# Kernel optimization log

Hardware: AMD Instinct MI355X
Metric: run time of the kernel (lower is better)

Reference implementation:

```python
import jax, jax.numpy as jnp
import numpy as np

B, T, S, C = 4096, 128, 16, 128
NEG = -1e30  # finite stand-in for -inf to keep grads NaN-free


def setup_inputs() -> dict:
    key = jax.random.key(0)
    k1, k2 = jax.random.split(key)
    prediction = jax.random.normal(k1, (B, T, C), dtype=jnp.float32)  # treated as log-probs, as in the original
    lable = jax.random.normal(k2, (B, S, C), dtype=jnp.float32)       # one-hot-ish label scores
    return {"prediction": prediction, "lable": lable}


def _ctc_nll(logp, targets):
    """CTC negative log-likelihood, full-length inputs/targets.
    logp: (B, T, C) log-probabilities, blank=0. targets: (B, S) int.
    Returns nll: (B,)."""
    Bb, Tt, Cc = logp.shape
    Ss = targets.shape[1]
    L = 2 * Ss + 1  # extended label: blank-interleaved
    neg = jnp.float32(NEG)

    ext = jnp.zeros((Bb, L), dtype=targets.dtype).at[:, 1::2].set(targets)
    # skip transition l-2 -> l allowed iff ext[l] != ext[l-2] (auto-false on blanks)
    skip_ok = jnp.concatenate(
        [jnp.zeros((Bb, 2), dtype=bool), ext[:, 2:] != ext[:, :-2]], axis=1)

    # gather log-probs of extended labels for every time step: (B, T, L)
    logp_ext = jnp.take_along_axis(logp, ext[:, None, :], axis=2)

    alpha0 = (jnp.full((Bb, L), neg)
              .at[:, 0].set(logp_ext[:, 0, 0])
              .at[:, 1].set(logp_ext[:, 0, 1]))

    pad1 = jnp.full((Bb, 1), neg)
    pad2 = jnp.full((Bb, 2), neg)

    def step(alpha, lp_t):
        a1 = alpha
        a2 = jnp.concatenate([pad1, alpha[:, :-1]], axis=1)
        a3 = jnp.where(skip_ok, jnp.concatenate([pad2, alpha[:, :-2]], axis=1), neg)
        alpha_new = jnp.logaddexp(jnp.logaddexp(a1, a2), a3) + lp_t
        return alpha_new, None

    alpha_T, _ = jax.lax.scan(step, alpha0, jnp.swapaxes(logp_ext, 0, 1)[1:])
    nll = -jnp.logaddexp(alpha_T[:, -1], alpha_T[:, -2])
    return nll


def reference(prediction, lable):
    # synthesize_lable: per-(b,s) argmax over classes -> integer targets (B, S)
    targets = jnp.argmax(lable, axis=-1)
    nll = _ctc_nll(prediction, targets)
    # zero_infinity=True
    nll = jnp.where(jnp.isfinite(nll), nll, jnp.float32(0.0))
    # reduction='mean': divide each loss by its target length, then batch-mean
    Ss = lable.shape[1]
    return jnp.mean(nll / jnp.float32(Ss))
```

## Files before the change

### kernel.cpp

```cpp
#include <hip/hip_runtime.h>
#include <math.h>
#include <stdint.h>

#define B_ 4096
#define T_ 128
#define S_ 16
#define C_ 128
#define L_ 33
#define NSLOT 17
#define NELEM (T_ * NSLOT)
#define LDSF  (NELEM + 64)
#define NWAVE 2048
#define NEGV (-1e30f)
#define LOG2E 1.4426950408889634f
#define LN2 0.6931471805599453f
#define NEGB (NEGV * LOG2E)

__device__ __forceinline__ float hexp2(float x) { return __builtin_amdgcn_exp2f(x); }
__device__ __forceinline__ float hlog2(float x) { return __builtin_amdgcn_logf(x); }

__device__ __forceinline__ unsigned fkey(float v) {
    unsigned u = __float_as_uint(v);
    return (u & 0x80000000u) ? ~u : (u | 0x80000000u);
}

typedef const __attribute__((address_space(1))) unsigned int* gas_t;
typedef __attribute__((address_space(3))) unsigned int* las_t;

__global__ __launch_bounds__(256) void ctc_main_kernel(
        const float* __restrict__ pred,
        const float* __restrict__ lab,
        float* __restrict__ out_b) {
    const int wid  = threadIdx.x >> 6;
    const int lane = threadIdx.x & 63;
    const int w = blockIdx.x * 4 + wid;
    const int b0 = w, b1 = w + NWAVE;

    __shared__ int   cls_tab[4][NSLOT];
    __shared__ float lps[4][LDSF];
    int*   mytab = cls_tab[wid];
    float* mylds = lps[wid];

    const int half = lane >> 5;
    const int li   = lane & 31;

    const int l = lane;
    int cidx = 0;
    if (l < L_ && (l & 1)) cidx = 1 + ((l - 1) >> 1);
    const bool has2 = (l >= 1);
    const bool odd3 = (l < L_ && (l & 1) && l >= 3);

    float4 q[8];
    auto load_lab = [&](int b) {
        const float4* lr = (const float4*)(lab + (size_t)b * S_ * C_ + (size_t)half * C_);
        #pragma unroll
        for (int sp = 0; sp < 8; ++sp)
            q[sp] = lr[(size_t)sp * 2 * (C_ / 4) + li];
    };
    auto argmax_tab = [&]() {
        if (lane == 0) mytab[0] = 0;
        #pragma unroll
        for (int sp = 0; sp < 8; ++sp) {
            float vals[4] = {q[sp].x, q[sp].y, q[sp].z, q[sp].w};
            unsigned long long key = 0;
            #pragma unroll
            for (int k = 0; k < 4; ++k) {
                unsigned long long kk =
                    ((unsigned long long)fkey(vals[k]) << 32) | (unsigned)(~(li * 4 + k));
                if (kk > key) key = kk;
            }
            #pragma unroll
            for (int off = 16; off >= 1; off >>= 1) {
                unsigned long long ok = __shfl_xor(key, off, 64);
                if (ok > key) key = ok;
            }
            if (li == 0) mytab[1 + sp * 2 + half] = (int)(~(unsigned)key) & 127;
        }
        asm volatile("s_waitcnt lgkmcnt(0)" ::: "memory");
    };
    auto stage = [&](const float* pb, int i0, int i1) {
        for (int i = i0; i < i1; ++i) {
            unsigned e = i * 64 + lane;
            unsigned t = e / NSLOT;
            unsigned s = e - t * NSLOT;
            const float* src = pb + (size_t)t * C_ + mytab[s];
            __builtin_amdgcn_global_load_lds((gas_t)src, (las_t)(mylds + i * 64), 4, 0, 0);
        }
        __builtin_amdgcn_sched_barrier(0);
    };

    float beta, lpA, lpB, lpC;
    bool skipv;
    auto ring_init = [&]() {
        beta = (l <= 1) ? mylds[cidx] * LOG2E : NEGB;
        lpA = mylds[1 * NSLOT + cidx];
        lpB = mylds[2 * NSLOT + cidx];
        lpC = mylds[3 * NSLOT + cidx];
    };
#define SEG(T0, T1)                                                         \
    _Pragma("unroll 4")                                                     \
    for (int t = (T0); t <= (T1); ++t) {                                    \
        float lp = lpA; lpA = lpB; lpB = lpC;                               \
        lpC = mylds[(t + 3) * NSLOT + cidx];                                \
        float a2 = __shfl_up(beta, 1, 64);                                  \
        float a3 = __shfl_up(beta, 2, 64);                                  \
        a2 = has2  ? a2 : NEGB;                                             \
        a3 = skipv ? a3 : NEGB;                                             \
        float m = fmaxf(fmaxf(beta, a2), a3);                               \
        float s = hexp2(beta - m) + hexp2(a2 - m) + hexp2(a3 - m);          \
        beta = fmaf(lp, LOG2E, m + hlog2(s));                               \
    }
    auto finish = [&](int b) {
        float b31 = __shfl(beta, L_ - 2, 64);
        float b32 = __shfl(beta, L_ - 1, 64);
        float m2 = fmaxf(b31, b32);
        float nll = -(m2 + hlog2(hexp2(b31 - m2) + hexp2(b32 - m2))) * LN2;
        if (!isfinite(nll)) nll = 0.0f;
        if (lane == 0) out_b[b] = nll * (1.0f / (float)S_);
    };

    const float* pb0 = pred + (size_t)b0 * T_ * C_;
    const float* pb1 = pred + (size_t)b1 * T_ * C_;

    load_lab(b0);
    asm volatile("s_waitcnt vmcnt(0)" ::: "memory");
    argmax_tab();
    bool skip0 = odd3 && (mytab[cidx] != mytab[cidx - 1]);
    stage(pb0, 0, 17);
    stage(pb0, 17, 34);
    load_lab(b1);
    __builtin_amdgcn_sched_barrier(0);

    asm volatile("s_waitcnt vmcnt(25)" ::: "memory");
    ring_init();
    skipv = skip0;
    SEG(1, 60)

    asm volatile("s_waitcnt vmcnt(0)" ::: "memory");
    argmax_tab();
    bool skip1 = odd3 && (mytab[cidx] != mytab[cidx - 1]);
    stage(pb1, 0, 17);
    SEG(61, 127)
    finish(b0);

    stage(pb1, 17, 34);
    asm volatile("s_waitcnt vmcnt(17)" ::: "memory");
    ring_init();
    skipv = skip1;
    SEG(1, 60)

    asm volatile("s_waitcnt vmcnt(0)" ::: "memory");
    SEG(61, 127)
    finish(b1);
#undef SEG
}

__global__ __launch_bounds__(256) void reduce_mean_kernel(
        const float* __restrict__ in, float* __restrict__ out) {
    __shared__ float sm[256];
    const int tid = threadIdx.x;
    float v[16];
    #pragma unroll
    for (int i = 0; i < 16; ++i) v[i] = in[tid + i * 256];
    float s = 0.f;
    #pragma unroll
    for (int i = 0; i < 16; ++i) s += v[i];
    sm[tid] = s;
    __syncthreads();
    for (int w = 128; w >= 1; w >>= 1) {
        if (tid < w) sm[tid] += sm[tid + w];
        __syncthreads();
    }
    if (tid == 0) out[0] = sm[0] / (float)B_;
}

extern "C" void kernel_launch(void* const* d_in, const int* in_sizes, int n_in,
                              void* d_out, int out_size, void* d_ws, size_t ws_size,
                              hipStream_t stream) {
    const float* pred = (const float*)d_in[0];
    const float* lab  = (const float*)d_in[1];
    float* ws = (float*)d_ws;
    ctc_main_kernel<<<NWAVE / 4, 256, 0, stream>>>(pred, lab, ws);
    reduce_mean_kernel<<<1, 256, 0, stream>>>(ws, (float*)d_out);
}
```

Baseline: 65.81 us.

## Process one batch per wave with double-buffered chunked LDS staging

Each wave now handles a single batch instead of two, which doubles the grid to 4096 waves and raises per-SIMD occupancy for the latency-bound serial alpha recurrence. The full per-batch gathered log-prob table in LDS is replaced by a two-region ring of 32-timestep chunks, staged ahead of the compute loop. This roughly halves LDS per wave and permits launch_bounds(256,8). The trade-off is losing the old overlap of the second batch's label argmax and staging with the first batch's recurrence, and adding more per-chunk waitcnt points.

Measured after the change: 61.76 us. 1.07x faster.

```diff
diff --git a/kernel.cpp b/kernel.cpp
--- a/kernel.cpp
+++ b/kernel.cpp
@@ -8,9 +8,10 @@
 #define C_ 128
 #define L_ 33
 #define NSLOT 17
-#define NELEM (T_ * NSLOT)
-#define LDSF  (NELEM + 64)
-#define NWAVE 2048
+#define CH_ROWS 32
+#define CH_FLOATS 544
+#define REG_FLOATS 544
+#define LDS_FLOATS 1120
 #define NEGV (-1e30f)
 #define LOG2E 1.4426950408889634f
 #define LN2 0.6931471805599453f
@@ -27,41 +28,38 @@
 typedef const __attribute__((address_space(1))) unsigned int* gas_t;
 typedef __attribute__((address_space(3))) unsigned int* las_t;
 
-__global__ __launch_bounds__(256) void ctc_main_kernel(
+__global__ __launch_bounds__(256, 8) void ctc_main_kernel(
         const float* __restrict__ pred,
         const float* __restrict__ lab,
         float* __restrict__ out_b) {
     const int wid  = threadIdx.x >> 6;
     const int lane = threadIdx.x & 63;
-    const int w = blockIdx.x * 4 + wid;
-    const int b0 = w, b1 = w + NWAVE;
+    const int b = blockIdx.x * 4 + wid;
 
     __shared__ int   cls_tab[4][NSLOT];
-    __shared__ float lps[4][LDSF];
+    __shared__ float lps[4][LDS_FLOATS];
     int*   mytab = cls_tab[wid];
     float* mylds = lps[wid];
 
     const int half = lane >> 5;
     const int li   = lane & 31;
 
-    const int l = lane;
-    int cidx = 0;
-    if (l < L_ && (l & 1)) cidx = 1 + ((l - 1) >> 1);
-    const bool has2 = (l >= 1);
-    const bool odd3 = (l < L_ && (l & 1) && l >= 3);
-
-    float4 q[8];
-    auto load_lab = [&](int b) {
-        const float4* lr = (const float4*)(lab + (size_t)b * S_ * C_ + (size_t)half * C_);
+    const float4* lr =
+        (const float4*)(lab + (size_t)b * S_ * C_ + (size_t)half * C_);
+    if (lane == 0) mytab[0] = 0;
+    #pragma unroll
+    for (int pass = 0; pass < 2; ++pass) {
+        float4 q[4];
         #pragma unroll
-        for (int sp = 0; sp < 8; ++sp)
-            q[sp] = lr[(size_t)sp * 2 * (C_ / 4) + li];
-    };
-    auto argmax_tab = [&]() {
-        if (lane == 0) mytab[0] = 0;
+        for (int j = 0; j < 4; ++j) {
+            int sp = pass * 4 + j;
+            q[j] = lr[(size_t)sp * 2 * (C_ / 4) + li];
+        }
+        asm volatile("s_waitcnt vmcnt(0)" ::: "memory");
         #pragma unroll
-        for (int sp = 0; sp < 8; ++sp) {
-            float vals[4] = {q[sp].x, q[sp].y, q[sp].z, q[sp].w};
+        for (int j = 0; j < 4; ++j) {
+            int sp = pass * 4 + j;
+            float vals[4] = {q[j].x, q[j].y, q[j].z, q[j].w};
             unsigned long long key = 0;
             #pragma unroll
             for (int k = 0; k < 4; ++k) {
@@ -76,32 +74,42 @@
             }
             if (li == 0) mytab[1 + sp * 2 + half] = (int)(~(unsigned)key) & 127;
         }
-        asm volatile("s_waitcnt lgkmcnt(0)" ::: "memory");
-    };
-    auto stage = [&](const float* pb, int i0, int i1) {
-        for (int i = i0; i < i1; ++i) {
+    }
+    asm volatile("s_waitcnt lgkmcnt(0)" ::: "memory");
+
+    const int l = lane;
+    int cidx = 0;
+    if (l < L_ && (l & 1)) cidx = 1 + ((l - 1) >> 1);
+    const bool has2 = (l >= 1);
+    const bool skipv =
+        (l < L_ && (l & 1) && l >= 3) && (mytab[cidx] != mytab[cidx - 1]);
+
+    const float* pb = pred + (size_t)b * T_ * C_;
+
+    auto stage_chunk = [&](int c) {
+        const int roff = (c & 1) * REG_FLOATS;
+        #pragma unroll
+        for (int i = 0; i < 9; ++i) {
             unsigned e = i * 64 + lane;
-            unsigned t = e / NSLOT;
-            unsigned s = e - t * NSLOT;
-            const float* src = pb + (size_t)t * C_ + mytab[s];
-            __builtin_amdgcn_global_load_lds((gas_t)src, (las_t)(mylds + i * 64), 4, 0, 0);
+            if (i < 8 || lane < 32) {
+                unsigned tl = e / NSLOT;
+                unsigned s  = e - tl * NSLOT;
+                const float* src = pb + (size_t)(c * CH_ROWS + tl) * C_ + mytab[s];
+                __builtin_amdgcn_global_load_lds((gas_t)src,
+                                                 (las_t)(mylds + roff + e), 4, 0, 0);
+            }
         }
         __builtin_amdgcn_sched_barrier(0);
     };
 
+#define LPOFF(tt) (((((tt) >> 5) & 1) * REG_FLOATS) + (((tt) & 31) * NSLOT) + cidx)
+
     float beta, lpA, lpB, lpC;
-    bool skipv;
-    auto ring_init = [&]() {
-        beta = (l <= 1) ? mylds[cidx] * LOG2E : NEGB;
-        lpA = mylds[1 * NSLOT + cidx];
-        lpB = mylds[2 * NSLOT + cidx];
-        lpC = mylds[3 * NSLOT + cidx];
-    };
 #define SEG(T0, T1)                                                         \
     _Pragma("unroll 4")                                                     \
     for (int t = (T0); t <= (T1); ++t) {                                    \
         float lp = lpA; lpA = lpB; lpB = lpC;                               \
-        lpC = mylds[(t + 3) * NSLOT + cidx];                                \
+        lpC = mylds[LPOFF(t + 3)];                                          \
         float a2 = __shfl_up(beta, 1, 64);                                  \
         float a3 = __shfl_up(beta, 2, 64);                                  \
         a2 = has2  ? a2 : NEGB;                                             \
@@ -110,49 +118,34 @@
         float s = hexp2(beta - m) + hexp2(a2 - m) + hexp2(a3 - m);          \
         beta = fmaf(lp, LOG2E, m + hlog2(s));                               \
     }
-    auto finish = [&](int b) {
-        float b31 = __shfl(beta, L_ - 2, 64);
-        float b32 = __shfl(beta, L_ - 1, 64);
-        float m2 = fmaxf(b31, b32);
-        float nll = -(m2 + hlog2(hexp2(b31 - m2) + hexp2(b32 - m2))) * LN2;
-        if (!isfinite(nll)) nll = 0.0f;
-        if (lane == 0) out_b[b] = nll * (1.0f / (float)S_);
-    };
 
-    const float* pb0 = pred + (size_t)b0 * T_ * C_;
-    const float* pb1 = pred + (size_t)b1 * T_ * C_;
+    stage_chunk(0);
+    stage_chunk(1);
+    asm volatile("s_waitcnt vmcnt(9)" ::: "memory");
 
-    load_lab(b0);
+    beta = (l <= 1) ? mylds[cidx] * LOG2E : NEGB;
+    lpA = mylds[LPOFF(1)];
+    lpB = mylds[LPOFF(2)];
+    lpC = mylds[LPOFF(3)];
+
+    SEG(1, 28)
+    stage_chunk(2);
+    asm volatile("s_waitcnt vmcnt(9)" ::: "memory");
+    SEG(29, 60)
+    stage_chunk(3);
+    asm volatile("s_waitcnt vmcnt(9)" ::: "memory");
+    SEG(61, 92)
     asm volatile("s_waitcnt vmcnt(0)" ::: "memory");
-    argmax_tab();
-    bool skip0 = odd3 && (mytab[cidx] != mytab[cidx - 1]);
-    stage(pb0, 0, 17);
-    stage(pb0, 17, 34);
-    load_lab(b1);
-    __builtin_amdgcn_sched_barrier(0);
+    SEG(93, 127)
+#undef SEG
+#undef LPOFF
 
-    asm volatile("s_waitcnt vmcnt(25)" ::: "memory");
-    ring_init();
-    skipv = skip0;
-    SEG(1, 60)
-
-    asm volatile("s_waitcnt vmcnt(0)" ::: "memory");
-    argmax_tab();
-    bool skip1 = odd3 && (mytab[cidx] != mytab[cidx - 1]);
-    stage(pb1, 0, 17);
-    SEG(61, 127)
-    finish(b0);
-
-    stage(pb1, 17, 34);
-    asm volatile("s_waitcnt vmcnt(17)" ::: "memory");
-    ring_init();
-    skipv = skip1;
-    SEG(1, 60)
-
-    asm volatile("s_waitcnt vmcnt(0)" ::: "memory");
-    SEG(61, 127)
-    finish(b1);
-#undef SEG
+    float b31 = __shfl(beta, L_ - 2, 64);
+    float b32 = __shfl(beta, L_ - 1, 64);
+    float m2 = fmaxf(b31, b32);
+    float nll = -(m2 + hlog2(hexp2(b31 - m2) + hexp2(b32 - m2))) * LN2;
+    if (!isfinite(nll)) nll = 0.0f;
+    if (lane == 0) out_b[b] = nll * (1.0f / (float)S_);
 }
 
 __global__ __launch_bounds__(256) void reduce_mean_kernel(
@@ -180,6 +173,6 @@
     const float* pred = (const float*)d_in[0];
     const float* lab  = (const float*)d_in[1];
     float* ws = (float*)d_ws;
-    ctc_main_kernel<<<NWAVE / 4, 256, 0, stream>>>(pred, lab, ws);
+    ctc_main_kernel<<<B_ / 4, 256, 0, stream>>>(pred, lab, ws);
     reduce_mean_kernel<<<1, 256, 0, stream>>>(ws, (float*)d_out);
 }
```
